# Kernel tuning notes

Measured on AMD Instinct MI355X. Metric: run time of the kernel, lower is better.

The kernel has to match this reference:

```python
import jax, jax.numpy as jnp
import numpy as np

B, S, E = 2, 2048, 1024
H, HKV = 16, 4
D = E // H          # head_dim = 64
REP = H // HKV      # kv repeat factor = 4


def setup_inputs() -> dict:
    key = jax.random.key(0)
    ks = jax.random.split(key, 9)
    std = 0.02
    x = jax.random.normal(ks[0], (B, S, E), dtype=jnp.float32)
    # causal mask: True means masked (upper triangle, strictly above diagonal)
    mask = jnp.triu(jnp.ones((S, S), dtype=bool), k=1)
    wq_w = jax.random.normal(ks[1], (E, E), dtype=jnp.float32) * std
    wq_b = jax.random.normal(ks[2], (E,), dtype=jnp.float32) * std
    wk_w = jax.random.normal(ks[3], (HKV * D, E), dtype=jnp.float32) * std
    wk_b = jax.random.normal(ks[4], (HKV * D,), dtype=jnp.float32) * std
    wv_w = jax.random.normal(ks[5], (HKV * D, E), dtype=jnp.float32) * std
    wv_b = jax.random.normal(ks[6], (HKV * D,), dtype=jnp.float32) * std
    wo_w = jax.random.normal(ks[7], (E, E), dtype=jnp.float32) * std
    wo_b = jax.random.normal(ks[8], (E,), dtype=jnp.float32) * std
    return {"x": x, "mask": mask, "wq_w": wq_w, "wq_b": wq_b,
            "wk_w": wk_w, "wk_b": wk_b, "wv_w": wv_w, "wv_b": wv_b,
            "wo_w": wo_w, "wo_b": wo_b}


def reference(x, mask, wq_w, wq_b, wk_w, wk_b, wv_w, wv_b, wo_w, wo_b):
    b, s, e = x.shape
    # projections (torch Linear: x @ W.T + b)
    q = x @ wq_w.T + wq_b                       # [B,S,E]
    k = x @ wk_w.T + wk_b                       # [B,S,HKV*D]
    v = x @ wv_w.T + wv_b
    # q grouped by kv head: [B, HKV, REP, S, D]; k/v: [B, HKV, S, D]
    q = q.reshape(b, s, HKV, REP, D).transpose(0, 2, 3, 1, 4)
    k = k.reshape(b, s, HKV, D).transpose(0, 2, 1, 3)
    v = v.reshape(b, s, HKV, D).transpose(0, 2, 1, 3)
    scale = D ** (-0.5)
    # scores [B, HKV, REP, Sq, Skv] -- same math as physical repeat_kv
    scores = jnp.einsum('bgrsd,bgtd->bgrst', q, k) * scale
    scores = jnp.where(mask, -jnp.inf, scores)
    w = jax.nn.softmax(scores, axis=-1)
    ctx = jnp.einsum('bgrst,bgtd->bgrsd', w, v)  # [B,HKV,REP,S,D]
    ctx = ctx.transpose(0, 3, 1, 2, 4).reshape(b, s, e)
    return ctx @ wo_w.T + wo_b
```

## Files before the change

kernel.cpp:

```cpp
#include <hip/hip_runtime.h>


typedef __attribute__((ext_vector_type(8))) short bh8;
typedef __attribute__((ext_vector_type(4))) short sh4;
typedef __attribute__((ext_vector_type(4))) float fv4;
typedef __attribute__((ext_vector_type(2))) unsigned int uv2;

#define MFMA16 __builtin_amdgcn_mfma_f32_16x16x32_bf16

static __device__ __forceinline__ float fast_exp2(float x) {
  return __builtin_amdgcn_exp2f(x);
}
static __device__ __forceinline__ unsigned short f2bf(float f) {
  unsigned int u; __builtin_memcpy(&u, &f, 4);
  u += 0x7fffu + ((u >> 16) & 1u);
  return (unsigned short)(u >> 16);
}
static __device__ __forceinline__ unsigned int pack2(float a, float b) {
  return (unsigned int)(unsigned short)f2bf(a) |
         ((unsigned int)(unsigned short)f2bf(b) << 16);
}
static __device__ __forceinline__ void gload16(const short* g, short* l) {
  __builtin_amdgcn_global_load_lds(
      (const __attribute__((address_space(1))) void*)g,
      (__attribute__((address_space(3))) void*)l, 16, 0, 0);
}

static __device__ __forceinline__ bh8 pshuf(const float* p, int quad, int l16) {
  unsigned int u01 = pack2(p[0], p[1]);
  unsigned int u23 = pack2(p[2], p[3]);
  unsigned int u45 = pack2(p[4], p[5]);
  unsigned int u67 = pack2(p[6], p[7]);
  const int g0 = (((quad << 1)    ) & 3) * 16 + l16;
  const int g1 = (((quad << 1) + 1) & 3) * 16 + l16;
  unsigned int w0l = __shfl((int)u01, g0), w0h = __shfl((int)u45, g0);
  unsigned int w1l = __shfl((int)u23, g0), w1h = __shfl((int)u67, g0);
  unsigned int w2l = __shfl((int)u01, g1), w2h = __shfl((int)u45, g1);
  unsigned int w3l = __shfl((int)u23, g1), w3h = __shfl((int)u67, g1);
  const bool up = (quad & 2) != 0;
  union { unsigned int w[4]; bh8 v; } pu;
  pu.w[0] = up ? w0h : w0l;
  pu.w[1] = up ? w1h : w1l;
  pu.w[2] = up ? w2h : w2l;
  pu.w[3] = up ? w3h : w3l;
  return pu.v;
}

__global__ __launch_bounds__(256) void cvt_all(
    const float* __restrict__ x,  const float* __restrict__ wq,
    const float* __restrict__ wk, const float* __restrict__ wv,
    const float* __restrict__ wo,
    short* __restrict__ xb, short* __restrict__ wqkvb, short* __restrict__ wob)
{
  const int i = blockIdx.x * 256 + threadIdx.x;
  const float* src; short* dst; int j;
  if (i < 1048576)      { j = i;           src = x;  dst = xb; }
  else if (i < 1310720) { j = i - 1048576; src = wq; dst = wqkvb; }
  else if (i < 1376256) { j = i - 1310720; src = wk; dst = wqkvb + (size_t)1024 * 1024; }
  else if (i < 1441792) { j = i - 1376256; src = wv; dst = wqkvb + (size_t)1280 * 1024; }
  else                  { j = i - 1441792; src = wo; dst = wob; }
  const float4 v = ((const float4*)src)[j];
  sh4 o = { (short)f2bf(v.x), (short)f2bf(v.y),
            (short)f2bf(v.z), (short)f2bf(v.w) };
  ((sh4*)dst)[j] = o;
}

__global__ __launch_bounds__(256) void gemm_dbuf(
    const short* __restrict__ A, const short* __restrict__ W,
    const float* __restrict__ biasQ, const float* __restrict__ biasK,
    const float* __restrict__ biasV,
    short* __restrict__ Cq, short* __restrict__ Ck, short* __restrict__ Cvt,
    float* __restrict__ Cf,
    int M, int K, int S, int mode, float scaleQ)
{
  __shared__ short As[2][128 * 32];
  __shared__ short Bs[2][64 * 32];
  const int tid  = threadIdx.x;
  const int wave = tid >> 6, lane = tid & 63;
  const int quad = lane >> 4, l16 = lane & 15;
  const int row0 = blockIdx.x * 128, col0 = blockIdx.y * 64;
  const int wr = (wave >> 1) * 64, wc = (wave & 1) * 32;

  fv4 acc[4][2] = {};

  const int srow = wave * 16 + (lane >> 2);
  const int skp  = (lane & 3) * 8;
  const short* ag = A + (size_t)(row0 + srow) * K + skp;
  const short* bg = W + (size_t)(col0 + srow) * K + skp;

  auto stage = [&](int b, int k0) {
    gload16(ag + k0,                  &As[b][(wave * 16) * 32]);
    gload16(ag + (size_t)64 * K + k0, &As[b][(64 + wave * 16) * 32]);
    gload16(bg + k0,                  &Bs[b][(wave * 16) * 32]);
  };

  stage(0, 0);
  __syncthreads();
  const int nIter = K / 32;
  for (int it = 0; it < nIter; it++) {
    const int cur = it & 1;
    if (it + 1 < nIter) stage(cur ^ 1, (it + 1) * 32);

    bh8 af[4], bf[2];
    #pragma unroll
    for (int i = 0; i < 4; i++)
      af[i] = *(const bh8*)&As[cur][(wr + i * 16 + l16) * 32 + quad * 8];
    #pragma unroll
    for (int j = 0; j < 2; j++)
      bf[j] = *(const bh8*)&Bs[cur][(wc + j * 16 + l16) * 32 + quad * 8];
    #pragma unroll
    for (int i = 0; i < 4; i++)
      #pragma unroll
      for (int j = 0; j < 2; j++)
        acc[i][j] = MFMA16(af[i], bf[j], acc[i][j], 0, 0, 0);
    __syncthreads();
  }

  if (mode == 2) {
    float bv[2];
    #pragma unroll
    for (int j = 0; j < 2; j++) bv[j] = biasQ[col0 + wc + j * 16 + l16];
    #pragma unroll
    for (int i = 0; i < 4; i++) {
      const int row = row0 + wr + i * 16 + quad * 4;
      #pragma unroll
      for (int j = 0; j < 2; j++) {
        const int col = col0 + wc + j * 16 + l16;
        #pragma unroll
        for (int r = 0; r < 4; r++)
          Cf[(size_t)(row + r) * 1024 + col] = acc[i][j][r] + bv[j];
      }
    }
  } else if (col0 < 1024) {
    float bv[2];
    #pragma unroll
    for (int j = 0; j < 2; j++) bv[j] = biasQ[col0 + wc + j * 16 + l16];
    #pragma unroll
    for (int i = 0; i < 4; i++) {
      const int row = row0 + wr + i * 16 + quad * 4;
      #pragma unroll
      for (int j = 0; j < 2; j++) {
        const int col = col0 + wc + j * 16 + l16;
        #pragma unroll
        for (int r = 0; r < 4; r++)
          Cq[(size_t)(row + r) * 1024 + col] =
              (short)f2bf((acc[i][j][r] + bv[j]) * scaleQ);
      }
    }
  } else if (col0 < 1280) {
    float bv[2];
    #pragma unroll
    for (int j = 0; j < 2; j++) bv[j] = biasK[col0 + wc + j * 16 + l16 - 1024];
    #pragma unroll
    for (int i = 0; i < 4; i++) {
      const int row = row0 + wr + i * 16 + quad * 4;
      #pragma unroll
      for (int j = 0; j < 2; j++) {
        const int col = col0 + wc + j * 16 + l16 - 1024;
        #pragma unroll
        for (int r = 0; r < 4; r++)
          Ck[(size_t)(row + r) * 256 + col] = (short)f2bf(acc[i][j][r] + bv[j]);
      }
    }
  } else {
    float bv[2];
    #pragma unroll
    for (int j = 0; j < 2; j++) bv[j] = biasV[col0 + wc + j * 16 + l16 - 1280];
    const int b  = row0 / S;
    const int sb = row0 - b * S;
    #pragma unroll
    for (int i = 0; i < 4; i++) {
      const int s = sb + wr + i * 16 + quad * 4;
      #pragma unroll
      for (int j = 0; j < 2; j++) {
        const int np = col0 + wc + j * 16 + l16 - 1280;
        sh4 v = { (short)f2bf(acc[i][j][0] + bv[j]),
                  (short)f2bf(acc[i][j][1] + bv[j]),
                  (short)f2bf(acc[i][j][2] + bv[j]),
                  (short)f2bf(acc[i][j][3] + bv[j]) };
        *(sh4*)(Cvt + ((size_t)(b * 256 + np)) * S + s) = v;
      }
    }
  }
}

__global__ __launch_bounds__(256) void gqa_attn(
    const short* __restrict__ Q,
    const short* __restrict__ Kg,
    const short* __restrict__ Vt,
    short* __restrict__ ctx)
{
  const int S = 2048, E = 1024, KVE = 256;
  __shared__ short Ks[2][4096];
  __shared__ short Vs[2][4096];
  __shared__ short P2[4][16 * 72];

  const int wave = threadIdx.x >> 6;
  const int lane = threadIdx.x & 63;
  const int quad = lane >> 4, l16 = lane & 15;
  const int bh = blockIdx.y;
  const int b = bh >> 4, h = bh & 15, kv = h >> 2;

  const short* Kb = Kg + (size_t)b * S * KVE + kv * 64;
  const short* Vb = Vt + ((size_t)(b * 4 + kv)) * 64 * S;
  short* Pw = &P2[wave][0];

  const int srow = lane >> 3;
  const int scg  = (lane & 7) ^ srow;

  const int kc0 = (quad ^ (l16 & 7)) * 8;
  const int kc1 = ((quad ^ 4) ^ (l16 & 7)) * 8;
  const int pwr = l16 * 72;

  auto stageKV = [&](int buf, int t0) {
    #pragma unroll
    for (int e = 0; e < 2; e++) {
      const int g = wave * 2 + e;
      const int row = g * 8 + srow;
      gload16(Kb + (size_t)(t0 + row) * KVE + scg * 8, &Ks[buf][g * 512]);
      gload16(Vb + (size_t)row * S + t0 + scg * 8,     &Vs[buf][g * 512]);
    }
  };

  for (int ph = 0; ph < 2; ph++) {
    const int j = ph ? (31 - (int)blockIdx.x) : (int)blockIdx.x;
    const int qblk0 = j * 64;
    const int q0 = qblk0 + wave * 16;

    const short* qrow = Q + (size_t)(b * S + q0 + l16) * E + h * 64 + quad * 8;
    bh8 qf0 = *(const bh8*)(qrow);
    bh8 qf1 = *(const bh8*)(qrow + 32);

    fv4 acc0{}, acc1{}, acc2{}, acc3{};
    float rs = 0.f;

    const int nInt = qblk0 >> 6;
    if (nInt > 0) {
      stageKV(0, 0);
      __syncthreads();
      for (int it = 0; it < nInt; it++) {
        const int cur = it & 1;
        if (it + 1 < nInt) stageKV(cur ^ 1, (it + 1) * 64);

        fv4 st[4] = {};
        #pragma unroll
        for (int i = 0; i < 4; i++) {
          const int tb = (i * 16 + l16) * 64;
          bh8 k0 = *(const bh8*)&Ks[cur][tb + kc0];
          bh8 k1 = *(const bh8*)&Ks[cur][tb + kc1];
          st[i] = MFMA16(k0, qf0, st[i], 0, 0, 0);
          st[i] = MFMA16(k1, qf1, st[i], 0, 0, 0);
        }
        #pragma unroll
        for (int i = 0; i < 4; i++) {
          float p0 = fast_exp2(st[i][0]);
          float p1 = fast_exp2(st[i][1]);
          float p2 = fast_exp2(st[i][2]);
          float p3 = fast_exp2(st[i][3]);
          rs += (p0 + p1) + (p2 + p3);
          uv2 u = { pack2(p0, p1), pack2(p2, p3) };
          *(uv2*)&Pw[pwr + i * 16 + quad * 4] = u;
        }
        bh8 pfA = *(const bh8*)&Pw[pwr + quad * 8];
        bh8 pfB = *(const bh8*)&Pw[pwr + 32 + quad * 8];
        #pragma unroll
        for (int dt = 0; dt < 4; dt++) {
          const int db = (dt * 16 + l16) * 64;
          bh8 v0 = *(const bh8*)&Vs[cur][db + kc0];
          bh8 v1 = *(const bh8*)&Vs[cur][db + kc1];
          fv4* a = dt == 0 ? &acc0 : dt == 1 ? &acc1 : dt == 2 ? &acc2 : &acc3;
          *a = MFMA16(v0, pfA, *a, 0, 0, 0);
          *a = MFMA16(v1, pfB, *a, 0, 0, 0);
        }
        __syncthreads();
      }
    }

    const int nk = q0 + 16;
    for (int t0 = qblk0; t0 < nk; t0 += 32) {
      fv4 st0{}, st1{};
      {
        const short* kr = Kb + (size_t)(t0 + l16) * KVE + quad * 8;
        bh8 k0 = *(const bh8*)(kr);
        bh8 k1 = *(const bh8*)(kr + 32);
        st0 = MFMA16(k0, qf0, st0, 0, 0, 0);
        st0 = MFMA16(k1, qf1, st0, 0, 0, 0);
      }
      const bool do2 = (t0 + 16) < nk;
      if (do2) {
        const short* kr = Kb + (size_t)(t0 + 16 + l16) * KVE + quad * 8;
        bh8 k0 = *(const bh8*)(kr);
        bh8 k1 = *(const bh8*)(kr + 32);
        st1 = MFMA16(k0, qf0, st1, 0, 0, 0);
        st1 = MFMA16(k1, qf1, st1, 0, 0, 0);
      }
      const int qg = q0 + l16;
      float p[8];
      #pragma unroll
      for (int r = 0; r < 4; r++) {
        const int t = t0 + quad * 4 + r;
        p[r]     = (t <= qg)               ? fast_exp2(st0[r]) : 0.f;
        p[4 + r] = (do2 && (t + 16) <= qg) ? fast_exp2(st1[r]) : 0.f;
      }
      #pragma unroll
      for (int i = 0; i < 8; i++) rs += p[i];

      bh8 pf = pshuf(p, quad, l16);
      const short* vr = Vb + (size_t)l16 * S + t0 + quad * 8;
      acc0 = MFMA16(*(const bh8*)(vr),          pf, acc0, 0, 0, 0);
      acc1 = MFMA16(*(const bh8*)(vr + 16 * S), pf, acc1, 0, 0, 0);
      acc2 = MFMA16(*(const bh8*)(vr + 32 * S), pf, acc2, 0, 0, 0);
      acc3 = MFMA16(*(const bh8*)(vr + 48 * S), pf, acc3, 0, 0, 0);
    }

    float lsum = rs;
    lsum += __shfl_xor(lsum, 16);
    lsum += __shfl_xor(lsum, 32);
    const float inv = 1.f / lsum;

    short* orow = ctx + (size_t)(b * S + q0 + l16) * E + h * 64 + quad * 4;
    sh4 o0 = { (short)f2bf(acc0[0] * inv), (short)f2bf(acc0[1] * inv),
               (short)f2bf(acc0[2] * inv), (short)f2bf(acc0[3] * inv) };
    sh4 o1 = { (short)f2bf(acc1[0] * inv), (short)f2bf(acc1[1] * inv),
               (short)f2bf(acc1[2] * inv), (short)f2bf(acc1[3] * inv) };
    sh4 o2 = { (short)f2bf(acc2[0] * inv), (short)f2bf(acc2[1] * inv),
               (short)f2bf(acc2[2] * inv), (short)f2bf(acc2[3] * inv) };
    sh4 o3 = { (short)f2bf(acc3[0] * inv), (short)f2bf(acc3[1] * inv),
               (short)f2bf(acc3[2] * inv), (short)f2bf(acc3[3] * inv) };
    *(sh4*)(orow)      = o0;
    *(sh4*)(orow + 16) = o1;
    *(sh4*)(orow + 32) = o2;
    *(sh4*)(orow + 48) = o3;
  }
}

extern "C" void kernel_launch(void* const* d_in, const int* in_sizes, int n_in,
                              void* d_out, int out_size, void* d_ws, size_t ws_size,
                              hipStream_t stream)
{
  const float* x    = (const float*)d_in[0];
  const float* wq_w = (const float*)d_in[2];
  const float* wq_b = (const float*)d_in[3];
  const float* wk_w = (const float*)d_in[4];
  const float* wk_b = (const float*)d_in[5];
  const float* wv_w = (const float*)d_in[6];
  const float* wv_b = (const float*)d_in[7];
  const float* wo_w = (const float*)d_in[8];
  const float* wo_b = (const float*)d_in[9];
  float* out = (float*)d_out;

  const int S = 2048, E = 1024, M = 2 * S;
  const float sl2e = 0.125f * 1.44269504f;

  char* ob = (char*)d_out;
  short* Qb   = (short*)(ob);
  short* Kbuf = (short*)(ob + (size_t)( 8 << 20));
  short* Vtb  = (short*)(ob + (size_t)(10 << 20));

  char* ws = (char*)d_ws;
  short* xb    = (short*)(ws);
  short* wqkvb = (short*)(ws + (size_t)( 8 << 20));
  short* wob   = (short*)(ws + (size_t)(11 << 20));
  short* Cx    = xb;

  dim3 blk(256);
  cvt_all<<<dim3(6656), blk, 0, stream>>>(x, wq_w, wk_w, wv_w, wo_w,
                                          xb, wqkvb, wob);
  gemm_dbuf<<<dim3(M / 128, 1536 / 64), blk, 0, stream>>>(
      xb, wqkvb, wq_b, wk_b, wv_b, Qb, Kbuf, Vtb, nullptr, M, E, S, 0, sl2e);
  gqa_attn<<<dim3(16, 2 * 16), blk, 0, stream>>>(Qb, Kbuf, Vtb, Cx);
  gemm_dbuf<<<dim3(M / 128, 1024 / 64), blk, 0, stream>>>(
      Cx, wob, wo_b, nullptr, nullptr, nullptr, nullptr, nullptr, out,
      M, E, S, 2, 1.f);
}
```

Before: 180.1 us.

## Launch one attention block per query tile, load K/V directly from global

The attention kernel previously paired two query tiles per block (j and 31-j) for causal load balancing and staged K/V through double-buffered LDS via global_load_lds with barriers. It now launches 32 blocks per head, each handling one tile in reverse order, and reads K and V fragments straight from global memory with no shared staging or __syncthreads. pack2 also switches to the hardware v_cvt_pk_bf16_f32 instruction. This doubles the grid and drops barrier and LDS overhead, but the four waves in a block no longer share K/V reuse through LDS, so more traffic goes to the caches, and per-block work is now uneven across tiles.

```diff
diff --git a/kernel.cpp b/kernel.cpp
--- a/kernel.cpp
+++ b/kernel.cpp
@@ -17,8 +17,9 @@
   return (unsigned short)(u >> 16);
 }
 static __device__ __forceinline__ unsigned int pack2(float a, float b) {
-  return (unsigned int)(unsigned short)f2bf(a) |
-         ((unsigned int)(unsigned short)f2bf(b) << 16);
+  unsigned int r;
+  asm("v_cvt_pk_bf16_f32 %0, %1, %2" : "=v"(r) : "v"(a), "v"(b));
+  return r;
 }
 static __device__ __forceinline__ void gload16(const short* g, short* l) {
   __builtin_amdgcn_global_load_lds(
@@ -191,8 +192,6 @@
     short* __restrict__ ctx)
 {
   const int S = 2048, E = 1024, KVE = 256;
-  __shared__ short Ks[2][4096];
-  __shared__ short Vs[2][4096];
   __shared__ short P2[4][16 * 72];
 
   const int wave = threadIdx.x >> 6;
@@ -204,134 +203,107 @@
   const short* Kb = Kg + (size_t)b * S * KVE + kv * 64;
   const short* Vb = Vt + ((size_t)(b * 4 + kv)) * 64 * S;
   short* Pw = &P2[wave][0];
-
-  const int srow = lane >> 3;
-  const int scg  = (lane & 7) ^ srow;
-
-  const int kc0 = (quad ^ (l16 & 7)) * 8;
-  const int kc1 = ((quad ^ 4) ^ (l16 & 7)) * 8;
   const int pwr = l16 * 72;
 
-  auto stageKV = [&](int buf, int t0) {
-    #pragma unroll
-    for (int e = 0; e < 2; e++) {
-      const int g = wave * 2 + e;
-      const int row = g * 8 + srow;
-      gload16(Kb + (size_t)(t0 + row) * KVE + scg * 8, &Ks[buf][g * 512]);
-      gload16(Vb + (size_t)row * S + t0 + scg * 8,     &Vs[buf][g * 512]);
-    }
-  };
-
-  for (int ph = 0; ph < 2; ph++) {
-    const int j = ph ? (31 - (int)blockIdx.x) : (int)blockIdx.x;
-    const int qblk0 = j * 64;
-    const int q0 = qblk0 + wave * 16;
-
-    const short* qrow = Q + (size_t)(b * S + q0 + l16) * E + h * 64 + quad * 8;
-    bh8 qf0 = *(const bh8*)(qrow);
-    bh8 qf1 = *(const bh8*)(qrow + 32);
-
-    fv4 acc0{}, acc1{}, acc2{}, acc3{};
-    float rs = 0.f;
-
-    const int nInt = qblk0 >> 6;
-    if (nInt > 0) {
-      stageKV(0, 0);
-      __syncthreads();
-      for (int it = 0; it < nInt; it++) {
-        const int cur = it & 1;
-        if (it + 1 < nInt) stageKV(cur ^ 1, (it + 1) * 64);
-
-        fv4 st[4] = {};
-        #pragma unroll
-        for (int i = 0; i < 4; i++) {
-          const int tb = (i * 16 + l16) * 64;
-          bh8 k0 = *(const bh8*)&Ks[cur][tb + kc0];
-          bh8 k1 = *(const bh8*)&Ks[cur][tb + kc1];
-          st[i] = MFMA16(k0, qf0, st[i], 0, 0, 0);
-          st[i] = MFMA16(k1, qf1, st[i], 0, 0, 0);
-        }
-        #pragma unroll
-        for (int i = 0; i < 4; i++) {
-          float p0 = fast_exp2(st[i][0]);
-          float p1 = fast_exp2(st[i][1]);
-          float p2 = fast_exp2(st[i][2]);
-          float p3 = fast_exp2(st[i][3]);
-          rs += (p0 + p1) + (p2 + p3);
-          uv2 u = { pack2(p0, p1), pack2(p2, p3) };
-          *(uv2*)&Pw[pwr + i * 16 + quad * 4] = u;
-        }
-        bh8 pfA = *(const bh8*)&Pw[pwr + quad * 8];
-        bh8 pfB = *(const bh8*)&Pw[pwr + 32 + quad * 8];
-        #pragma unroll
-        for (int dt = 0; dt < 4; dt++) {
-          const int db = (dt * 16 + l16) * 64;
-          bh8 v0 = *(const bh8*)&Vs[cur][db + kc0];
-          bh8 v1 = *(const bh8*)&Vs[cur][db + kc1];
-          fv4* a = dt == 0 ? &acc0 : dt == 1 ? &acc1 : dt == 2 ? &acc2 : &acc3;
-          *a = MFMA16(v0, pfA, *a, 0, 0, 0);
-          *a = MFMA16(v1, pfB, *a, 0, 0, 0);
-        }
-        __syncthreads();
-      }
-    }
-
-    const int nk = q0 + 16;
-    for (int t0 = qblk0; t0 < nk; t0 += 32) {
-      fv4 st0{}, st1{};
-      {
-        const short* kr = Kb + (size_t)(t0 + l16) * KVE + quad * 8;
-        bh8 k0 = *(const bh8*)(kr);
-        bh8 k1 = *(const bh8*)(kr + 32);
-        st0 = MFMA16(k0, qf0, st0, 0, 0, 0);
-        st0 = MFMA16(k1, qf1, st0, 0, 0, 0);
-      }
-      const bool do2 = (t0 + 16) < nk;
-      if (do2) {
-        const short* kr = Kb + (size_t)(t0 + 16 + l16) * KVE + quad * 8;
-        bh8 k0 = *(const bh8*)(kr);
-        bh8 k1 = *(const bh8*)(kr + 32);
-        st1 = MFMA16(k0, qf0, st1, 0, 0, 0);
-        st1 = MFMA16(k1, qf1, st1, 0, 0, 0);
-      }
-      const int qg = q0 + l16;
-      float p[8];
-      #pragma unroll
-      for (int r = 0; r < 4; r++) {
-        const int t = t0 + quad * 4 + r;
-        p[r]     = (t <= qg)               ? fast_exp2(st0[r]) : 0.f;
-        p[4 + r] = (do2 && (t + 16) <= qg) ? fast_exp2(st1[r]) : 0.f;
-      }
-      #pragma unroll
-      for (int i = 0; i < 8; i++) rs += p[i];
-
-      bh8 pf = pshuf(p, quad, l16);
-      const short* vr = Vb + (size_t)l16 * S + t0 + quad * 8;
-      acc0 = MFMA16(*(const bh8*)(vr),          pf, acc0, 0, 0, 0);
-      acc1 = MFMA16(*(const bh8*)(vr + 16 * S), pf, acc1, 0, 0, 0);
-      acc2 = MFMA16(*(const bh8*)(vr + 32 * S), pf, acc2, 0, 0, 0);
-      acc3 = MFMA16(*(const bh8*)(vr + 48 * S), pf, acc3, 0, 0, 0);
-    }
-
-    float lsum = rs;
-    lsum += __shfl_xor(lsum, 16);
-    lsum += __shfl_xor(lsum, 32);
-    const float inv = 1.f / lsum;
-
-    short* orow = ctx + (size_t)(b * S + q0 + l16) * E + h * 64 + quad * 4;
-    sh4 o0 = { (short)f2bf(acc0[0] * inv), (short)f2bf(acc0[1] * inv),
-               (short)f2bf(acc0[2] * inv), (short)f2bf(acc0[3] * inv) };
-    sh4 o1 = { (short)f2bf(acc1[0] * inv), (short)f2bf(acc1[1] * inv),
-               (short)f2bf(acc1[2] * inv), (short)f2bf(acc1[3] * inv) };
-    sh4 o2 = { (short)f2bf(acc2[0] * inv), (short)f2bf(acc2[1] * inv),
-               (short)f2bf(acc2[2] * inv), (short)f2bf(acc2[3] * inv) };
-    sh4 o3 = { (short)f2bf(acc3[0] * inv), (short)f2bf(acc3[1] * inv),
-               (short)f2bf(acc3[2] * inv), (short)f2bf(acc3[3] * inv) };
-    *(sh4*)(orow)      = o0;
-    *(sh4*)(orow + 16) = o1;
-    *(sh4*)(orow + 32) = o2;
-    *(sh4*)(orow + 48) = o3;
+  const int j = 31 - (int)blockIdx.x;
+  const int qblk0 = j * 64;
+  const int q0 = qblk0 + wave * 16;
+
+  const short* qrow = Q + (size_t)(b * S + q0 + l16) * E + h * 64 + quad * 8;
+  bh8 qf0 = *(const bh8*)(qrow);
+  bh8 qf1 = *(const bh8*)(qrow + 32);
+
+  fv4 acc0{}, acc1{}, acc2{}, acc3{};
+  float rs = 0.f;
+
+  for (int t0 = 0; t0 < qblk0; t0 += 64) {
+    fv4 st[4] = {};
+    #pragma unroll
+    for (int i = 0; i < 4; i++) {
+      const short* kr = Kb + (size_t)(t0 + i * 16 + l16) * KVE + quad * 8;
+      bh8 k0 = *(const bh8*)(kr);
+      bh8 k1 = *(const bh8*)(kr + 32);
+      st[i] = MFMA16(k0, qf0, st[i], 0, 0, 0);
+      st[i] = MFMA16(k1, qf1, st[i], 0, 0, 0);
+    }
+    #pragma unroll
+    for (int i = 0; i < 4; i++) {
+      float p0 = fast_exp2(st[i][0]);
+      float p1 = fast_exp2(st[i][1]);
+      float p2 = fast_exp2(st[i][2]);
+      float p3 = fast_exp2(st[i][3]);
+      rs += (p0 + p1) + (p2 + p3);
+      uv2 u = { pack2(p0, p1), pack2(p2, p3) };
+      *(uv2*)&Pw[pwr + i * 16 + quad * 4] = u;
+    }
+    bh8 pfA = *(const bh8*)&Pw[pwr + quad * 8];
+    bh8 pfB = *(const bh8*)&Pw[pwr + 32 + quad * 8];
+    #pragma unroll
+    for (int dt = 0; dt < 4; dt++) {
+      const short* vr = Vb + (size_t)(dt * 16 + l16) * S + t0 + quad * 8;
+      bh8 v0 = *(const bh8*)(vr);
+      bh8 v1 = *(const bh8*)(vr + 32);
+      fv4* a = dt == 0 ? &acc0 : dt == 1 ? &acc1 : dt == 2 ? &acc2 : &acc3;
+      *a = MFMA16(v0, pfA, *a, 0, 0, 0);
+      *a = MFMA16(v1, pfB, *a, 0, 0, 0);
+    }
   }
+
+  const int nk = q0 + 16;
+  for (int t0 = qblk0; t0 < nk; t0 += 32) {
+    fv4 st0{}, st1{};
+    {
+      const short* kr = Kb + (size_t)(t0 + l16) * KVE + quad * 8;
+      bh8 k0 = *(const bh8*)(kr);
+      bh8 k1 = *(const bh8*)(kr + 32);
+      st0 = MFMA16(k0, qf0, st0, 0, 0, 0);
+      st0 = MFMA16(k1, qf1, st0, 0, 0, 0);
+    }
+    const bool do2 = (t0 + 16) < nk;
+    if (do2) {
+      const short* kr = Kb + (size_t)(t0 + 16 + l16) * KVE + quad * 8;
+      bh8 k0 = *(const bh8*)(kr);
+      bh8 k1 = *(const bh8*)(kr + 32);
+      st1 = MFMA16(k0, qf0, st1, 0, 0, 0);
+      st1 = MFMA16(k1, qf1, st1, 0, 0, 0);
+    }
+    const int qg = q0 + l16;
+    float p[8];
+    #pragma unroll
+    for (int r = 0; r < 4; r++) {
+      const int t = t0 + quad * 4 + r;
+      p[r]     = (t <= qg)               ? fast_exp2(st0[r]) : 0.f;
+      p[4 + r] = (do2 && (t + 16) <= qg) ? fast_exp2(st1[r]) : 0.f;
+    }
+    #pragma unroll
+    for (int i = 0; i < 8; i++) rs += p[i];
+
+    bh8 pf = pshuf(p, quad, l16);
+    const short* vr = Vb + (size_t)l16 * S + t0 + quad * 8;
+    acc0 = MFMA16(*(const bh8*)(vr),          pf, acc0, 0, 0, 0);
+    acc1 = MFMA16(*(const bh8*)(vr + 16 * S), pf, acc1, 0, 0, 0);
+    acc2 = MFMA16(*(const bh8*)(vr + 32 * S), pf, acc2, 0, 0, 0);
+    acc3 = MFMA16(*(const bh8*)(vr + 48 * S), pf, acc3, 0, 0, 0);
+  }
+
+  float lsum = rs;
+  lsum += __shfl_xor(lsum, 16);
+  lsum += __shfl_xor(lsum, 32);
+  const float inv = 1.f / lsum;
+
+  short* orow = ctx + (size_t)(b * S + q0 + l16) * E + h * 64 + quad * 4;
+  sh4 o0 = { (short)f2bf(acc0[0] * inv), (short)f2bf(acc0[1] * inv),
+             (short)f2bf(acc0[2] * inv), (short)f2bf(acc0[3] * inv) };
+  sh4 o1 = { (short)f2bf(acc1[0] * inv), (short)f2bf(acc1[1] * inv),
+             (short)f2bf(acc1[2] * inv), (short)f2bf(acc1[3] * inv) };
+  sh4 o2 = { (short)f2bf(acc2[0] * inv), (short)f2bf(acc2[1] * inv),
+             (short)f2bf(acc2[2] * inv), (short)f2bf(acc2[3] * inv) };
+  sh4 o3 = { (short)f2bf(acc3[0] * inv), (short)f2bf(acc3[1] * inv),
+             (short)f2bf(acc3[2] * inv), (short)f2bf(acc3[3] * inv) };
+  *(sh4*)(orow)      = o0;
+  *(sh4*)(orow + 16) = o1;
+  *(sh4*)(orow + 32) = o2;
+  *(sh4*)(orow + 48) = o3;
 }
 
 extern "C" void kernel_launch(void* const* d_in, const int* in_sizes, int n_in,
@@ -368,7 +340,7 @@
                                           xb, wqkvb, wob);
   gemm_dbuf<<<dim3(M / 128, 1536 / 64), blk, 0, stream>>>(
       xb, wqkvb, wq_b, wk_b, wv_b, Qb, Kbuf, Vtb, nullptr, M, E, S, 0, sl2e);
-  gqa_attn<<<dim3(16, 2 * 16), blk, 0, stream>>>(Qb, Kbuf, Vtb, Cx);
+  gqa_attn<<<dim3(32, 2 * 16), blk, 0, stream>>>(Qb, Kbuf, Vtb, Cx);
   gemm_dbuf<<<dim3(M / 128, 1024 / 64), blk, 0, stream>>>(
       Cx, wob, wo_b, nullptr, nullptr, nullptr, nullptr, nullptr, out,
       M, E, S, 2, 1.f);
```

Result: slower. 359.6 us (+99.6%).

## Deepen GEMM K-tile to 64 with XOR-swizzled LDS and hardware bf16 pack

Applied to the files above, without the earlier changes.

The projection GEMM now stages 64-wide K tiles instead of 32, which halves the number of barrier-separated iterations. The LDS layout is XOR-swizzled by row so the wider rows can be read without bank conflicts. pack2 now uses the v_cvt_pk_bf16_f32 instruction in place of software rounding. The cost is double the LDS footprint per block, which may reduce occupancy, and the hardware conversion may round differently from the old software path.

```diff
diff --git a/kernel.cpp b/kernel.cpp
--- a/kernel.cpp
+++ b/kernel.cpp
@@ -17,8 +17,9 @@
   return (unsigned short)(u >> 16);
 }
 static __device__ __forceinline__ unsigned int pack2(float a, float b) {
-  return (unsigned int)(unsigned short)f2bf(a) |
-         ((unsigned int)(unsigned short)f2bf(b) << 16);
+  unsigned int r;
+  asm("v_cvt_pk_bf16_f32 %0, %1, %2" : "=v"(r) : "v"(a), "v"(b));
+  return r;
 }
 static __device__ __forceinline__ void gload16(const short* g, short* l) {
   __builtin_amdgcn_global_load_lds(
@@ -73,8 +74,8 @@
     float* __restrict__ Cf,
     int M, int K, int S, int mode, float scaleQ)
 {
-  __shared__ short As[2][128 * 32];
-  __shared__ short Bs[2][64 * 32];
+  __shared__ short As[2][128 * 64];
+  __shared__ short Bs[2][64 * 64];
   const int tid  = threadIdx.x;
   const int wave = tid >> 6, lane = tid & 63;
   const int quad = lane >> 4, l16 = lane & 15;
@@ -83,36 +84,47 @@
 
   fv4 acc[4][2] = {};
 
-  const int srow = wave * 16 + (lane >> 2);
-  const int skp  = (lane & 3) * 8;
-  const short* ag = A + (size_t)(row0 + srow) * K + skp;
-  const short* bg = W + (size_t)(col0 + srow) * K + skp;
+  const int srow = lane >> 3;
+  const int scg  = (lane & 7) ^ srow;
+  const short* ag = A + (size_t)(row0 + wave * 32 + srow) * K + scg * 8;
+  const short* bg = W + (size_t)(col0 + wave * 16 + srow) * K + scg * 8;
 
   auto stage = [&](int b, int k0) {
-    gload16(ag + k0,                  &As[b][(wave * 16) * 32]);
-    gload16(ag + (size_t)64 * K + k0, &As[b][(64 + wave * 16) * 32]);
-    gload16(bg + k0,                  &Bs[b][(wave * 16) * 32]);
+    #pragma unroll
+    for (int e = 0; e < 4; e++)
+      gload16(ag + (size_t)(e * 8) * K + k0, &As[b][(wave * 32 + e * 8) * 64]);
+    #pragma unroll
+    for (int e = 0; e < 2; e++)
+      gload16(bg + (size_t)(e * 8) * K + k0, &Bs[b][(wave * 16 + e * 8) * 64]);
   };
 
   stage(0, 0);
   __syncthreads();
-  const int nIter = K / 32;
+  const int nIter = K / 64;
   for (int it = 0; it < nIter; it++) {
     const int cur = it & 1;
-    if (it + 1 < nIter) stage(cur ^ 1, (it + 1) * 32);
-
-    bh8 af[4], bf[2];
-    #pragma unroll
-    for (int i = 0; i < 4; i++)
-      af[i] = *(const bh8*)&As[cur][(wr + i * 16 + l16) * 32 + quad * 8];
-    #pragma unroll
-    for (int j = 0; j < 2; j++)
-      bf[j] = *(const bh8*)&Bs[cur][(wc + j * 16 + l16) * 32 + quad * 8];
-    #pragma unroll
-    for (int i = 0; i < 4; i++)
-      #pragma unroll
-      for (int j = 0; j < 2; j++)
-        acc[i][j] = MFMA16(af[i], bf[j], acc[i][j], 0, 0, 0);
+    if (it + 1 < nIter) stage(cur ^ 1, (it + 1) * 64);
+
+    #pragma unroll
+    for (int kk = 0; kk < 2; kk++) {
+      const int g = kk * 4 + quad;
+      bh8 af[4], bf[2];
+      #pragma unroll
+      for (int i = 0; i < 4; i++) {
+        const int r = wr + i * 16 + l16;
+        af[i] = *(const bh8*)&As[cur][r * 64 + ((g ^ (r & 7)) * 8)];
+      }
+      #pragma unroll
+      for (int j = 0; j < 2; j++) {
+        const int r = wc + j * 16 + l16;
+        bf[j] = *(const bh8*)&Bs[cur][r * 64 + ((g ^ (r & 7)) * 8)];
+      }
+      #pragma unroll
+      for (int i = 0; i < 4; i++)
+        #pragma unroll
+        for (int j = 0; j < 2; j++)
+          acc[i][j] = MFMA16(af[i], bf[j], acc[i][j], 0, 0, 0);
+    }
     __syncthreads();
   }
 
```

After: 170.6 us. 1.06x faster.
